# Kernel optimization log

Measured on AMD Instinct MI355X. Metric: run time of the kernel, lower is better.

Reference implementation:

```python
import jax, jax.numpy as jnp
import numpy as np

N_NODES = 100000


def _gcn_propagate(x, src, dst, n):
    """Symmetric-normalized propagation with self-loops (PyG gcn_norm, K=1).

    out[dst] += deg^-1/2[src] * deg^-1/2[dst] * x[src], including self-loops.
    """
    loop = jnp.arange(n, dtype=src.dtype)
    s = jnp.concatenate([src, loop])
    d = jnp.concatenate([dst, loop])
    deg = jax.ops.segment_sum(jnp.ones_like(d, dtype=x.dtype), d, num_segments=n)
    dinv = jnp.where(deg > 0, jax.lax.rsqrt(deg), jnp.zeros_like(deg))
    norm = dinv[s] * dinv[d]            # [E+N]
    msg = x[s] * norm[:, None]          # [E+N, F] gathered messages
    return jax.ops.segment_sum(msg, d, num_segments=n)


def setup_inputs() -> dict:
    key = jax.random.key(0)
    ks = jax.random.split(key, 6)
    n, e, f, h, c = N_NODES, 1600000, 64, 64, 16
    x = jax.random.normal(ks[0], (n, f), dtype=jnp.float32)
    edge_index = jax.random.randint(ks[1], (2, e), 0, n, dtype=jnp.int64)
    W1 = jax.random.normal(ks[2], (h, f), dtype=jnp.float32) * 0.1
    b1 = jnp.zeros((h,), dtype=jnp.float32)
    W2 = jax.random.normal(ks[3], (h, h), dtype=jnp.float32) * 0.1
    b2 = jnp.zeros((h,), dtype=jnp.float32)
    W3 = jax.random.normal(ks[4], (c, h), dtype=jnp.float32) * 0.1
    b3 = jnp.zeros((c,), dtype=jnp.float32)
    return {"x": x, "edge_index": edge_index, "W1": W1, "b1": b1,
            "W2": W2, "b2": b2, "W3": W3, "b3": b3}


def reference(x, edge_index, W1, b1, W2, b2, W3, b3):
    n = x.shape[0]
    src, dst = edge_index[0], edge_index[1]
    # SGConv 1 (K=1): propagate then linear; dropout is identity in eval mode
    h = _gcn_propagate(x, src, dst, n) @ W1.T + b1
    h = jax.nn.relu(h)
    # SGConv 2
    h = _gcn_propagate(h, src, dst, n) @ W2.T + b2
    h = jax.nn.relu(h)
    # final linear
    return h @ W3.T + b3
```

## Files before the change

kernel.cpp:

```cpp
#include <hip/hip_runtime.h>
#include <hip/hip_fp16.h>


#define F 64
#define C 16
#define SCAN_B 1024

__device__ __forceinline__ float4 ld_h4(const float2* base, size_t idx) {
    float2 raw = base[idx];
    __half2 lo = __builtin_bit_cast(__half2, raw.x);
    __half2 hi = __builtin_bit_cast(__half2, raw.y);
    float2 f0 = __half22float2(lo);
    float2 f1 = __half22float2(hi);
    return make_float4(f0.x, f0.y, f1.x, f1.y);
}

__device__ __forceinline__ float rl(float v, int l) {
    return __uint_as_float(__builtin_amdgcn_readlane(__float_as_uint(v), l));
}

__global__ void degrank_kernel(const int* __restrict__ dst, int* __restrict__ deg,
                               int* __restrict__ rank, int E) {
    int i = (blockIdx.x * blockDim.x + threadIdx.x) * 4;
    if (i + 4 <= E) {
        int4 d = *(const int4*)(dst + i);
        rank[i]     = atomicAdd(&deg[d.x], 1);
        rank[i + 1] = atomicAdd(&deg[d.y], 1);
        rank[i + 2] = atomicAdd(&deg[d.z], 1);
        rank[i + 3] = atomicAdd(&deg[d.w], 1);
    } else {
        for (int k = i; k < E; ++k) rank[k] = atomicAdd(&deg[dst[k]], 1);
    }
}

__global__ __launch_bounds__(256) void scan1_kernel(const int* __restrict__ deg,
                                                    int* __restrict__ part,
                                                    int* __restrict__ bsum, int n) {
    __shared__ int ts[256];
    int b = blockIdx.x, t = threadIdx.x;
    int base = b * SCAN_B + t * 4;
    int v[4], sum = 0;
#pragma unroll
    for (int k = 0; k < 4; ++k) { int i = base + k; v[k] = (i < n) ? deg[i] : 0; sum += v[k]; }
    ts[t] = sum;
    __syncthreads();
    for (int off = 1; off < 256; off <<= 1) {
        int add = (t >= off) ? ts[t - off] : 0;
        __syncthreads();
        ts[t] += add;
        __syncthreads();
    }
    int run = ts[t] - sum;
#pragma unroll
    for (int k = 0; k < 4; ++k) { int i = base + k; if (i < n) part[i] = run; run += v[k]; }
    if (t == 255) bsum[b] = ts[255];
}

__global__ __launch_bounds__(256) void scan2_kernel(int* __restrict__ bsum, int nb) {
    __shared__ int ts[256];
    int t = threadIdx.x;
    int v = (t < nb) ? bsum[t] : 0;
    ts[t] = v;
    __syncthreads();
    for (int off = 1; off < 256; off <<= 1) {
        int add = (t >= off) ? ts[t - off] : 0;
        __syncthreads();
        ts[t] += add;
        __syncthreads();
    }
    if (t < nb) bsum[t] = ts[t] - v;
}

__global__ void scan3_kernel(const int* __restrict__ part, const int* __restrict__ bsum,
                             const int* __restrict__ deg, int* __restrict__ rowptr,
                             float* __restrict__ dinv, int n, int E) {
    int i = blockIdx.x * blockDim.x + threadIdx.x;
    if (i < n) {
        rowptr[i] = part[i] + bsum[i / SCAN_B];
        dinv[i] = rsqrtf((float)deg[i] + 1.0f);
    }
    if (i == 0) rowptr[n] = E;
}

__global__ void fill_kernel(const int* __restrict__ src, const int* __restrict__ dst,
                            const int* __restrict__ rank, const int* __restrict__ rowptr,
                            int* __restrict__ csr_src, int E) {
    int i = (blockIdx.x * blockDim.x + threadIdx.x) * 4;
    if (i + 4 <= E) {
        int4 s = *(const int4*)(src + i);
        int4 d = *(const int4*)(dst + i);
        int4 r = *(const int4*)(rank + i);
        csr_src[rowptr[d.x] + r.x] = s.x;
        csr_src[rowptr[d.y] + r.y] = s.y;
        csr_src[rowptr[d.z] + r.z] = s.z;
        csr_src[rowptr[d.w] + r.w] = s.w;
    } else {
        for (int k = i; k < E; ++k) csr_src[rowptr[dst[k]] + rank[k]] = src[k];
    }
}

template <bool SCALE>
__global__ __launch_bounds__(256) void gemm_kernel(
    const float4* __restrict__ in4, const float* __restrict__ W,
    const float* __restrict__ scale, __half* __restrict__ yout, int n) {
    int tid = threadIdx.x;
    int lane = tid & 63;
    int m = lane & 15;
    float4 w[16];
#pragma unroll
    for (int t = 0; t < 16; ++t) w[t] = *(const float4*)(W + (size_t)lane * F + 4 * t);
    int gw = blockIdx.x * 4 + (tid >> 6);
    int nw = gridDim.x * 4;
    int node = gw;
    if (node >= n) return;
    float4 v = in4[(size_t)node * 16 + m];
    while (true) {
        int nxt = node + nw;
        float4 vn;
        if (nxt < n) vn = in4[(size_t)nxt * 16 + m];
        float acc = 0.0f;
#pragma unroll
        for (int t = 0; t < 16; ++t) {
            acc = fmaf(rl(v.x, t), w[t].x, acc);
            acc = fmaf(rl(v.y, t), w[t].y, acc);
            acc = fmaf(rl(v.z, t), w[t].z, acc);
            acc = fmaf(rl(v.w, t), w[t].w, acc);
        }
        if (SCALE) acc *= scale[node];
        yout[(size_t)node * F + lane] = __float2half(acc);
        if (nxt >= n) break;
        v = vn;
        node = nxt;
    }
}

__global__ __launch_bounds__(256) void gather1_kernel(
    const float2* __restrict__ y, const int* __restrict__ rowptr,
    const int* __restrict__ csr_src, const float* __restrict__ dinv,
    const float* __restrict__ b1, float* __restrict__ h1s, int n) {
    int tid = threadIdx.x;
    int m = tid & 15;
    float4 bias = *(const float4*)(b1 + 4 * m);
    int qid = (blockIdx.x * 256 + tid) >> 4;
    int nq = (gridDim.x * 256) >> 4;
    for (int node = qid; node < n; node += nq) {
        int beg = rowptr[node], end = rowptr[node + 1];
        float4 a0 = {0, 0, 0, 0}, a1 = {0, 0, 0, 0}, a2 = {0, 0, 0, 0}, a3 = {0, 0, 0, 0};
        int p = beg;
        for (; p + 8 <= end; p += 8) {
            int s0 = csr_src[p],     s1 = csr_src[p + 1];
            int s2 = csr_src[p + 2], s3 = csr_src[p + 3];
            int s4 = csr_src[p + 4], s5 = csr_src[p + 5];
            int s6 = csr_src[p + 6], s7 = csr_src[p + 7];
            float4 v0 = ld_h4(y, (size_t)s0 * 16 + m);
            float4 v1 = ld_h4(y, (size_t)s1 * 16 + m);
            float4 v2 = ld_h4(y, (size_t)s2 * 16 + m);
            float4 v3 = ld_h4(y, (size_t)s3 * 16 + m);
            float4 v4 = ld_h4(y, (size_t)s4 * 16 + m);
            float4 v5 = ld_h4(y, (size_t)s5 * 16 + m);
            float4 v6 = ld_h4(y, (size_t)s6 * 16 + m);
            float4 v7 = ld_h4(y, (size_t)s7 * 16 + m);
            a0.x += v0.x + v4.x; a0.y += v0.y + v4.y; a0.z += v0.z + v4.z; a0.w += v0.w + v4.w;
            a1.x += v1.x + v5.x; a1.y += v1.y + v5.y; a1.z += v1.z + v5.z; a1.w += v1.w + v5.w;
            a2.x += v2.x + v6.x; a2.y += v2.y + v6.y; a2.z += v2.z + v6.z; a2.w += v2.w + v6.w;
            a3.x += v3.x + v7.x; a3.y += v3.y + v7.y; a3.z += v3.z + v7.z; a3.w += v3.w + v7.w;
        }
        if (p + 4 <= end) {
            int s0 = csr_src[p], s1 = csr_src[p + 1], s2 = csr_src[p + 2], s3 = csr_src[p + 3];
            float4 v0 = ld_h4(y, (size_t)s0 * 16 + m);
            float4 v1 = ld_h4(y, (size_t)s1 * 16 + m);
            float4 v2 = ld_h4(y, (size_t)s2 * 16 + m);
            float4 v3 = ld_h4(y, (size_t)s3 * 16 + m);
            a0.x += v0.x; a0.y += v0.y; a0.z += v0.z; a0.w += v0.w;
            a1.x += v1.x; a1.y += v1.y; a1.z += v1.z; a1.w += v1.w;
            a2.x += v2.x; a2.y += v2.y; a2.z += v2.z; a2.w += v2.w;
            a3.x += v3.x; a3.y += v3.y; a3.z += v3.z; a3.w += v3.w;
            p += 4;
        }
        for (; p < end; ++p) {
            int s = csr_src[p];
            float4 v = ld_h4(y, (size_t)s * 16 + m);
            a0.x += v.x; a0.y += v.y; a0.z += v.z; a0.w += v.w;
        }
        a0.x += a1.x + a2.x + a3.x;
        a0.y += a1.y + a2.y + a3.y;
        a0.z += a1.z + a2.z + a3.z;
        a0.w += a1.w + a2.w + a3.w;
        float dd = dinv[node];
        float4 self = ld_h4(y, (size_t)node * 16 + m);
        float4 r;
        r.x = dd * fmaxf(fmaf(dd, a0.x + self.x, bias.x), 0.0f);
        r.y = dd * fmaxf(fmaf(dd, a0.y + self.y, bias.y), 0.0f);
        r.z = dd * fmaxf(fmaf(dd, a0.z + self.z, bias.z), 0.0f);
        r.w = dd * fmaxf(fmaf(dd, a0.w + self.w, bias.w), 0.0f);
        *(float4*)(h1s + (size_t)node * F + 4 * m) = r;
    }
}

__global__ __launch_bounds__(256) void gather2_kernel(
    const float2* __restrict__ y, const int* __restrict__ rowptr,
    const int* __restrict__ csr_src, const float* __restrict__ dinv,
    const float* __restrict__ b2, const float* __restrict__ W3,
    const float* __restrict__ b3, float* __restrict__ out, int n) {
    int tid = threadIdx.x;
    int lane = tid & 63;
    int m = lane & 15;
    int qbase = lane & 48;
    float4 bias = *(const float4*)(b2 + 4 * m);
    float b3r = b3[m];
    int qid = (blockIdx.x * 256 + tid) >> 4;
    int nq = (gridDim.x * 256) >> 4;
    for (int node = qid; node < n; node += nq) {
        int beg = rowptr[node], end = rowptr[node + 1];
        float4 a0 = {0, 0, 0, 0}, a1 = {0, 0, 0, 0}, a2 = {0, 0, 0, 0}, a3 = {0, 0, 0, 0};
        int p = beg;
        for (; p + 8 <= end; p += 8) {
            int s0 = csr_src[p],     s1 = csr_src[p + 1];
            int s2 = csr_src[p + 2], s3 = csr_src[p + 3];
            int s4 = csr_src[p + 4], s5 = csr_src[p + 5];
            int s6 = csr_src[p + 6], s7 = csr_src[p + 7];
            float4 v0 = ld_h4(y, (size_t)s0 * 16 + m);
            float4 v1 = ld_h4(y, (size_t)s1 * 16 + m);
            float4 v2 = ld_h4(y, (size_t)s2 * 16 + m);
            float4 v3 = ld_h4(y, (size_t)s3 * 16 + m);
            float4 v4 = ld_h4(y, (size_t)s4 * 16 + m);
            float4 v5 = ld_h4(y, (size_t)s5 * 16 + m);
            float4 v6 = ld_h4(y, (size_t)s6 * 16 + m);
            float4 v7 = ld_h4(y, (size_t)s7 * 16 + m);
            a0.x += v0.x + v4.x; a0.y += v0.y + v4.y; a0.z += v0.z + v4.z; a0.w += v0.w + v4.w;
            a1.x += v1.x + v5.x; a1.y += v1.y + v5.y; a1.z += v1.z + v5.z; a1.w += v1.w + v5.w;
            a2.x += v2.x + v6.x; a2.y += v2.y + v6.y; a2.z += v2.z + v6.z; a2.w += v2.w + v6.w;
            a3.x += v3.x + v7.x; a3.y += v3.y + v7.y; a3.z += v3.z + v7.z; a3.w += v3.w + v7.w;
        }
        if (p + 4 <= end) {
            int s0 = csr_src[p], s1 = csr_src[p + 1], s2 = csr_src[p + 2], s3 = csr_src[p + 3];
            float4 v0 = ld_h4(y, (size_t)s0 * 16 + m);
            float4 v1 = ld_h4(y, (size_t)s1 * 16 + m);
            float4 v2 = ld_h4(y, (size_t)s2 * 16 + m);
            float4 v3 = ld_h4(y, (size_t)s3 * 16 + m);
            a0.x += v0.x; a0.y += v0.y; a0.z += v0.z; a0.w += v0.w;
            a1.x += v1.x; a1.y += v1.y; a1.z += v1.z; a1.w += v1.w;
            a2.x += v2.x; a2.y += v2.y; a2.z += v2.z; a2.w += v2.w;
            a3.x += v3.x; a3.y += v3.y; a3.z += v3.z; a3.w += v3.w;
            p += 4;
        }
        for (; p < end; ++p) {
            int s = csr_src[p];
            float4 v = ld_h4(y, (size_t)s * 16 + m);
            a0.x += v.x; a0.y += v.y; a0.z += v.z; a0.w += v.w;
        }
        a0.x += a1.x + a2.x + a3.x;
        a0.y += a1.y + a2.y + a3.y;
        a0.z += a1.z + a2.z + a3.z;
        a0.w += a1.w + a2.w + a3.w;
        float dd = dinv[node];
        float4 self = ld_h4(y, (size_t)node * 16 + m);
        float4 h;
        h.x = fmaxf(fmaf(dd, a0.x + self.x, bias.x), 0.0f);
        h.y = fmaxf(fmaf(dd, a0.y + self.y, bias.y), 0.0f);
        h.z = fmaxf(fmaf(dd, a0.z + self.z, bias.z), 0.0f);
        h.w = fmaxf(fmaf(dd, a0.w + self.w, bias.w), 0.0f);
        float acc = 0.0f;
#pragma unroll
        for (int t = 0; t < 16; ++t) {
            float4 wv = *(const float4*)(W3 + (size_t)m * F + 4 * t);
            float hx = __shfl(h.x, qbase + t);
            float hy = __shfl(h.y, qbase + t);
            float hz = __shfl(h.z, qbase + t);
            float hw = __shfl(h.w, qbase + t);
            acc = fmaf(hx, wv.x, fmaf(hy, wv.y, fmaf(hz, wv.z, fmaf(hw, wv.w, acc))));
        }
        out[(size_t)node * C + m] = acc + b3r;
    }
}

extern "C" void kernel_launch(void* const* d_in, const int* in_sizes, int n_in,
                              void* d_out, int out_size, void* d_ws, size_t ws_size,
                              hipStream_t stream) {
    const float* x  = (const float*)d_in[0];
    const int* edge = (const int*)d_in[1];
    const float* W1 = (const float*)d_in[2];
    const float* b1 = (const float*)d_in[3];
    const float* W2 = (const float*)d_in[4];
    const float* b2 = (const float*)d_in[5];
    const float* W3 = (const float*)d_in[6];
    const float* b3 = (const float*)d_in[7];
    float* out = (float*)d_out;

    int n = in_sizes[0] / F;
    int E = in_sizes[1] / 2;
    const int* src = edge;
    const int* dst = edge + E;

    int nb = (n + SCAN_B - 1) / SCAN_B;

    char* ws = (char*)d_ws;
    size_t o = 0;
    auto alloc = [&](size_t bytes) { char* p = ws + o; o += (bytes + 255) & ~(size_t)255; return p; };
    int*    deg     = (int*)   alloc((size_t)n * 4);
    int*    rank    = (int*)   alloc((size_t)E * 4);
    int*    part    = (int*)   alloc((size_t)n * 4);
    int*    bsum    = (int*)   alloc(256 * 4);
    int*    rowptr  = (int*)   alloc((size_t)(n + 1) * 4);
    int*    csr_src = (int*)   alloc((size_t)E * 4);
    float*  dinv    = (float*) alloc((size_t)n * 4);
    __half* y1      = (__half*)alloc((size_t)n * F * 2);
    float*  h1s     = (float*) alloc((size_t)n * F * 4);
    __half* y2      = y1;

    hipMemsetAsync(deg, 0, (size_t)n * 4, stream);
    degrank_kernel<<<(E / 4 + 255) / 256, 256, 0, stream>>>(dst, deg, rank, E);

    scan1_kernel<<<nb, 256, 0, stream>>>(deg, part, bsum, n);
    scan2_kernel<<<1, 256, 0, stream>>>(bsum, nb);
    scan3_kernel<<<(n + 255) / 256, 256, 0, stream>>>(part, bsum, deg, rowptr, dinv, n, E);

    gemm_kernel<true><<<2048, 256, 0, stream>>>((const float4*)x, W1, dinv, y1, n);

    fill_kernel<<<(E / 4 + 255) / 256, 256, 0, stream>>>(src, dst, rank, rowptr, csr_src, E);

    gather1_kernel<<<2048, 256, 0, stream>>>(
        (const float2*)y1, rowptr, csr_src, dinv, b1, h1s, n);

    gemm_kernel<false><<<2048, 256, 0, stream>>>((const float4*)h1s, W2, nullptr, y2, n);

    gather2_kernel<<<2048, 256, 0, stream>>>(
        (const float2*)y2, rowptr, csr_src, dinv, b2, W3, b3, out, n);
}
```

Baseline: 283.5 us.

## Fuse second GEMM into gather2 and store layer-1 output in fp16

```diff
diff --git a/kernel.cpp b/kernel.cpp
--- a/kernel.cpp
+++ b/kernel.cpp
@@ -5,6 +5,10 @@
 #define F 64
 #define C 16
 #define SCAN_B 1024
+
+__device__ __forceinline__ float rl(float v, int l) {
+    return __uint_as_float(__builtin_amdgcn_readlane(__float_as_uint(v), l));
+}
 
 __device__ __forceinline__ float4 ld_h4(const float2* base, size_t idx) {
     float2 raw = base[idx];
@@ -13,10 +17,6 @@
     float2 f0 = __half22float2(lo);
     float2 f1 = __half22float2(hi);
     return make_float4(f0.x, f0.y, f1.x, f1.y);
-}
-
-__device__ __forceinline__ float rl(float v, int l) {
-    return __uint_as_float(__builtin_amdgcn_readlane(__float_as_uint(v), l));
 }
 
 __global__ void degrank_kernel(const int* __restrict__ dst, int* __restrict__ deg,
@@ -99,8 +99,7 @@
     }
 }
 
-template <bool SCALE>
-__global__ __launch_bounds__(256) void gemm_kernel(
+__global__ __launch_bounds__(256) void gemm1_kernel(
     const float4* __restrict__ in4, const float* __restrict__ W,
     const float* __restrict__ scale, __half* __restrict__ yout, int n) {
     int tid = threadIdx.x;
@@ -126,7 +125,7 @@
             acc = fmaf(rl(v.z, t), w[t].z, acc);
             acc = fmaf(rl(v.w, t), w[t].w, acc);
         }
-        if (SCALE) acc *= scale[node];
+        acc *= scale[node];
         yout[(size_t)node * F + lane] = __float2half(acc);
         if (nxt >= n) break;
         v = vn;
@@ -137,7 +136,7 @@
 __global__ __launch_bounds__(256) void gather1_kernel(
     const float2* __restrict__ y, const int* __restrict__ rowptr,
     const int* __restrict__ csr_src, const float* __restrict__ dinv,
-    const float* __restrict__ b1, float* __restrict__ h1s, int n) {
+    const float* __restrict__ b1, __half* __restrict__ h1s, int n) {
     int tid = threadIdx.x;
     int m = tid & 15;
     float4 bias = *(const float4*)(b1 + 4 * m);
@@ -193,25 +192,41 @@
         r.y = dd * fmaxf(fmaf(dd, a0.y + self.y, bias.y), 0.0f);
         r.z = dd * fmaxf(fmaf(dd, a0.z + self.z, bias.z), 0.0f);
         r.w = dd * fmaxf(fmaf(dd, a0.w + self.w, bias.w), 0.0f);
-        *(float4*)(h1s + (size_t)node * F + 4 * m) = r;
+        __half2 lo = __float22half2_rn(make_float2(r.x, r.y));
+        __half2 hi = __float22half2_rn(make_float2(r.z, r.w));
+        float2 packed;
+        packed.x = __builtin_bit_cast(float, lo);
+        packed.y = __builtin_bit_cast(float, hi);
+        *(float2*)(h1s + (size_t)node * F + 4 * m) = packed;
     }
 }
 
 __global__ __launch_bounds__(256) void gather2_kernel(
     const float2* __restrict__ y, const int* __restrict__ rowptr,
     const int* __restrict__ csr_src, const float* __restrict__ dinv,
-    const float* __restrict__ b2, const float* __restrict__ W3,
-    const float* __restrict__ b3, float* __restrict__ out, int n) {
+    const float* __restrict__ W2, const float* __restrict__ b2,
+    const float* __restrict__ W3, const float* __restrict__ b3,
+    float* __restrict__ out, int n) {
     int tid = threadIdx.x;
     int lane = tid & 63;
-    int m = lane & 15;
+    int q = lane >> 4, m = lane & 15;
     int qbase = lane & 48;
-    float4 bias = *(const float4*)(b2 + 4 * m);
-    float b3r = b3[m];
-    int qid = (blockIdx.x * 256 + tid) >> 4;
-    int nq = (gridDim.x * 256) >> 4;
-    for (int node = qid; node < n; node += nq) {
-        int beg = rowptr[node], end = rowptr[node + 1];
+    float4 w2[16];
+#pragma unroll
+    for (int t = 0; t < 16; ++t) w2[t] = *(const float4*)(W2 + (size_t)lane * F + 4 * t);
+    float4 w3[4];
+#pragma unroll
+    for (int t = 0; t < 4; ++t) w3[t] = *(const float4*)(W3 + (size_t)m * F + 16 * q + 4 * t);
+    float b2r = b2[lane];
+    float b3v = b3[m];
+    int wid = (blockIdx.x * 256 + tid) >> 6;
+    int nwaves = (gridDim.x * 256) >> 6;
+    for (int nb = wid * 4; nb < n; nb += nwaves * 4) {
+        int node = nb + q;
+        bool act = node < n;
+        int beg = 0, end = 0;
+        float dd = 0.0f;
+        if (act) { beg = rowptr[node]; end = rowptr[node + 1]; dd = dinv[node]; }
         float4 a0 = {0, 0, 0, 0}, a1 = {0, 0, 0, 0}, a2 = {0, 0, 0, 0}, a3 = {0, 0, 0, 0};
         int p = beg;
         for (; p + 8 <= end; p += 8) {
@@ -253,24 +268,35 @@
         a0.y += a1.y + a2.y + a3.y;
         a0.z += a1.z + a2.z + a3.z;
         a0.w += a1.w + a2.w + a3.w;
-        float dd = dinv[node];
-        float4 self = ld_h4(y, (size_t)node * 16 + m);
-        float4 h;
-        h.x = fmaxf(fmaf(dd, a0.x + self.x, bias.x), 0.0f);
-        h.y = fmaxf(fmaf(dd, a0.y + self.y, bias.y), 0.0f);
-        h.z = fmaxf(fmaf(dd, a0.z + self.z, bias.z), 0.0f);
-        h.w = fmaxf(fmaf(dd, a0.w + self.w, bias.w), 0.0f);
-        float acc = 0.0f;
-#pragma unroll
-        for (int t = 0; t < 16; ++t) {
-            float4 wv = *(const float4*)(W3 + (size_t)m * F + 4 * t);
-            float hx = __shfl(h.x, qbase + t);
-            float hy = __shfl(h.y, qbase + t);
-            float hz = __shfl(h.z, qbase + t);
-            float hw = __shfl(h.w, qbase + t);
-            acc = fmaf(hx, wv.x, fmaf(hy, wv.y, fmaf(hz, wv.z, fmaf(hw, wv.w, acc))));
-        }
-        out[(size_t)node * C + m] = acc + b3r;
+        float4 t4 = {0, 0, 0, 0};
+        if (act) {
+            float4 self = ld_h4(y, (size_t)node * 16 + m);
+            t4.x = dd * (a0.x + self.x);
+            t4.y = dd * (a0.y + self.y);
+            t4.z = dd * (a0.z + self.z);
+            t4.w = dd * (a0.w + self.w);
+        }
+#pragma unroll
+        for (int qq = 0; qq < 4; ++qq) {
+            if (nb + qq >= n) break;
+            float z = b2r;
+#pragma unroll
+            for (int tt = 0; tt < 16; ++tt) {
+                z = fmaf(rl(t4.x, 16 * qq + tt), w2[tt].x, z);
+                z = fmaf(rl(t4.y, 16 * qq + tt), w2[tt].y, z);
+                z = fmaf(rl(t4.z, 16 * qq + tt), w2[tt].z, z);
+                z = fmaf(rl(t4.w, 16 * qq + tt), w2[tt].w, z);
+            }
+            float h2 = fmaxf(z, 0.0f);
+            const float* w3f = (const float*)w3;
+            float partial = 0.0f;
+#pragma unroll
+            for (int tt = 0; tt < 16; ++tt)
+                partial = fmaf(__shfl(h2, qbase + tt), w3f[tt], partial);
+            partial += __shfl_xor(partial, 16);
+            partial += __shfl_xor(partial, 32);
+            if (lane < 16) out[(size_t)(nb + qq) * C + lane] = partial + b3v;
+        }
     }
 }
 
@@ -305,8 +331,7 @@
     int*    csr_src = (int*)   alloc((size_t)E * 4);
     float*  dinv    = (float*) alloc((size_t)n * 4);
     __half* y1      = (__half*)alloc((size_t)n * F * 2);
-    float*  h1s     = (float*) alloc((size_t)n * F * 4);
-    __half* y2      = y1;
+    __half* h1s     = (__half*)alloc((size_t)n * F * 2);
 
     hipMemsetAsync(deg, 0, (size_t)n * 4, stream);
     degrank_kernel<<<(E / 4 + 255) / 256, 256, 0, stream>>>(dst, deg, rank, E);
@@ -315,15 +340,13 @@
     scan2_kernel<<<1, 256, 0, stream>>>(bsum, nb);
     scan3_kernel<<<(n + 255) / 256, 256, 0, stream>>>(part, bsum, deg, rowptr, dinv, n, E);
 
-    gemm_kernel<true><<<2048, 256, 0, stream>>>((const float4*)x, W1, dinv, y1, n);
+    gemm1_kernel<<<2048, 256, 0, stream>>>((const float4*)x, W1, dinv, y1, n);
 
     fill_kernel<<<(E / 4 + 255) / 256, 256, 0, stream>>>(src, dst, rank, rowptr, csr_src, E);
 
     gather1_kernel<<<2048, 256, 0, stream>>>(
         (const float2*)y1, rowptr, csr_src, dinv, b1, h1s, n);
 
-    gemm_kernel<false><<<2048, 256, 0, stream>>>((const float4*)h1s, W2, nullptr, y2, n);
-
     gather2_kernel<<<2048, 256, 0, stream>>>(
-        (const float2*)y2, rowptr, csr_src, dinv, b2, W3, b3, out, n);
-}
+        (const float2*)h1s, rowptr, csr_src, dinv, W2, b2, W3, b3, out, n);
+}
```

Result: faster. 269.6 us (-4.9%).

## Split gather1 features across block pairs and store h1 in fp16

Applied to the files above, without the earlier changes.

```diff
diff --git a/kernel.cpp b/kernel.cpp
--- a/kernel.cpp
+++ b/kernel.cpp
@@ -5,6 +5,10 @@
 #define F 64
 #define C 16
 #define SCAN_B 1024
+
+__device__ __forceinline__ float rl(float v, int l) {
+    return __uint_as_float(__builtin_amdgcn_readlane(__float_as_uint(v), l));
+}
 
 __device__ __forceinline__ float4 ld_h4(const float2* base, size_t idx) {
     float2 raw = base[idx];
@@ -15,8 +19,9 @@
     return make_float4(f0.x, f0.y, f1.x, f1.y);
 }
 
-__device__ __forceinline__ float rl(float v, int l) {
-    return __uint_as_float(__builtin_amdgcn_readlane(__float_as_uint(v), l));
+__device__ __forceinline__ float2 ld_h2(const unsigned int* base, size_t idx) {
+    unsigned int raw = base[idx];
+    return __half22float2(__builtin_bit_cast(__half2, raw));
 }
 
 __global__ void degrank_kernel(const int* __restrict__ dst, int* __restrict__ deg,
@@ -99,8 +104,7 @@
     }
 }
 
-template <bool SCALE>
-__global__ __launch_bounds__(256) void gemm_kernel(
+__global__ __launch_bounds__(256) void gemm1_kernel(
     const float4* __restrict__ in4, const float* __restrict__ W,
     const float* __restrict__ scale, __half* __restrict__ yout, int n) {
     int tid = threadIdx.x;
@@ -126,7 +130,7 @@
             acc = fmaf(rl(v.z, t), w[t].z, acc);
             acc = fmaf(rl(v.w, t), w[t].w, acc);
         }
-        if (SCALE) acc *= scale[node];
+        acc *= scale[node];
         yout[(size_t)node * F + lane] = __float2half(acc);
         if (nxt >= n) break;
         v = vn;
@@ -134,66 +138,99 @@
     }
 }
 
+__global__ __launch_bounds__(256) void gemm2_kernel(
+    const float2* __restrict__ in2, const float* __restrict__ W,
+    __half* __restrict__ yout, int n) {
+    int tid = threadIdx.x;
+    int lane = tid & 63;
+    int m = lane & 15;
+    float4 w[16];
+#pragma unroll
+    for (int t = 0; t < 16; ++t) w[t] = *(const float4*)(W + (size_t)lane * F + 4 * t);
+    int gw = blockIdx.x * 4 + (tid >> 6);
+    int nw = gridDim.x * 4;
+    int node = gw;
+    if (node >= n) return;
+    float4 v = ld_h4(in2, (size_t)node * 16 + m);
+    while (true) {
+        int nxt = node + nw;
+        float4 vn;
+        if (nxt < n) vn = ld_h4(in2, (size_t)nxt * 16 + m);
+        float acc = 0.0f;
+#pragma unroll
+        for (int t = 0; t < 16; ++t) {
+            acc = fmaf(rl(v.x, t), w[t].x, acc);
+            acc = fmaf(rl(v.y, t), w[t].y, acc);
+            acc = fmaf(rl(v.z, t), w[t].z, acc);
+            acc = fmaf(rl(v.w, t), w[t].w, acc);
+        }
+        yout[(size_t)node * F + lane] = __float2half(acc);
+        if (nxt >= n) break;
+        v = vn;
+        node = nxt;
+    }
+}
+
 __global__ __launch_bounds__(256) void gather1_kernel(
-    const float2* __restrict__ y, const int* __restrict__ rowptr,
+    const unsigned int* __restrict__ y, const int* __restrict__ rowptr,
     const int* __restrict__ csr_src, const float* __restrict__ dinv,
-    const float* __restrict__ b1, float* __restrict__ h1s, int n) {
+    const float* __restrict__ b1, unsigned int* __restrict__ h1s, int n) {
     int tid = threadIdx.x;
     int m = tid & 15;
-    float4 bias = *(const float4*)(b1 + 4 * m);
-    int qid = (blockIdx.x * 256 + tid) >> 4;
-    int nq = (gridDim.x * 256) >> 4;
+    int s = blockIdx.x & 1;
+    int g = blockIdx.x >> 1;
+    int fo = 16 * s + m;
+    float2 bias = *(const float2*)(b1 + 32 * s + 2 * m);
+    int qid = g * 16 + (tid >> 4);
+    int nq = (gridDim.x >> 1) << 4;
     for (int node = qid; node < n; node += nq) {
         int beg = rowptr[node], end = rowptr[node + 1];
-        float4 a0 = {0, 0, 0, 0}, a1 = {0, 0, 0, 0}, a2 = {0, 0, 0, 0}, a3 = {0, 0, 0, 0};
+        float2 a0 = {0, 0}, a1 = {0, 0}, a2 = {0, 0}, a3 = {0, 0};
         int p = beg;
         for (; p + 8 <= end; p += 8) {
             int s0 = csr_src[p],     s1 = csr_src[p + 1];
             int s2 = csr_src[p + 2], s3 = csr_src[p + 3];
             int s4 = csr_src[p + 4], s5 = csr_src[p + 5];
             int s6 = csr_src[p + 6], s7 = csr_src[p + 7];
-            float4 v0 = ld_h4(y, (size_t)s0 * 16 + m);
-            float4 v1 = ld_h4(y, (size_t)s1 * 16 + m);
-            float4 v2 = ld_h4(y, (size_t)s2 * 16 + m);
-            float4 v3 = ld_h4(y, (size_t)s3 * 16 + m);
-            float4 v4 = ld_h4(y, (size_t)s4 * 16 + m);
-            float4 v5 = ld_h4(y, (size_t)s5 * 16 + m);
-            float4 v6 = ld_h4(y, (size_t)s6 * 16 + m);
-            float4 v7 = ld_h4(y, (size_t)s7 * 16 + m);
-            a0.x += v0.x + v4.x; a0.y += v0.y + v4.y; a0.z += v0.z + v4.z; a0.w += v0.w + v4.w;
-            a1.x += v1.x + v5.x; a1.y += v1.y + v5.y; a1.z += v1.z + v5.z; a1.w += v1.w + v5.w;
-            a2.x += v2.x + v6.x; a2.y += v2.y + v6.y; a2.z += v2.z + v6.z; a2.w += v2.w + v6.w;
-            a3.x += v3.x + v7.x; a3.y += v3.y + v7.y; a3.z += v3.z + v7.z; a3.w += v3.w + v7.w;
+            float2 v0 = ld_h2(y, (size_t)s0 * 32 + fo);
+            float2 v1 = ld_h2(y, (size_t)s1 * 32 + fo);
+            float2 v2 = ld_h2(y, (size_t)s2 * 32 + fo);
+            float2 v3 = ld_h2(y, (size_t)s3 * 32 + fo);
+            float2 v4 = ld_h2(y, (size_t)s4 * 32 + fo);
+            float2 v5 = ld_h2(y, (size_t)s5 * 32 + fo);
+            float2 v6 = ld_h2(y, (size_t)s6 * 32 + fo);
+            float2 v7 = ld_h2(y, (size_t)s7 * 32 + fo);
+            a0.x += v0.x + v4.x; a0.y += v0.y + v4.y;
+            a1.x += v1.x + v5.x; a1.y += v1.y + v5.y;
+            a2.x += v2.x + v6.x; a2.y += v2.y + v6.y;
+            a3.x += v3.x + v7.x; a3.y += v3.y + v7.y;
         }
         if (p + 4 <= end) {
             int s0 = csr_src[p], s1 = csr_src[p + 1], s2 = csr_src[p + 2], s3 = csr_src[p + 3];
-            float4 v0 = ld_h4(y, (size_t)s0 * 16 + m);
-            float4 v1 = ld_h4(y, (size_t)s1 * 16 + m);
-            float4 v2 = ld_h4(y, (size_t)s2 * 16 + m);
-            float4 v3 = ld_h4(y, (size_t)s3 * 16 + m);
-            a0.x += v0.x; a0.y += v0.y; a0.z += v0.z; a0.w += v0.w;
-            a1.x += v1.x; a1.y += v1.y; a1.z += v1.z; a1.w += v1.w;
-            a2.x += v2.x; a2.y += v2.y; a2.z += v2.z; a2.w += v2.w;
-            a3.x += v3.x; a3.y += v3.y; a3.z += v3.z; a3.w += v3.w;
+            float2 v0 = ld_h2(y, (size_t)s0 * 32 + fo);
+            float2 v1 = ld_h2(y, (size_t)s1 * 32 + fo);
+            float2 v2 = ld_h2(y, (size_t)s2 * 32 + fo);
+            float2 v3 = ld_h2(y, (size_t)s3 * 32 + fo);
+            a0.x += v0.x; a0.y += v0.y;
+            a1.x += v1.x; a1.y += v1.y;
+            a2.x += v2.x; a2.y += v2.y;
+            a3.x += v3.x; a3.y += v3.y;
             p += 4;
         }
         for (; p < end; ++p) {
-            int s = csr_src[p];
-            float4 v = ld_h4(y, (size_t)s * 16 + m);
-            a0.x += v.x; a0.y += v.y; a0.z += v.z; a0.w += v.w;
+            int sv = csr_src[p];
+            float2 v = ld_h2(y, (size_t)sv * 32 + fo);
+            a0.x += v.x; a0.y += v.y;
         }
         a0.x += a1.x + a2.x + a3.x;
         a0.y += a1.y + a2.y + a3.y;
-        a0.z += a1.z + a2.z + a3.z;
-        a0.w += a1.w + a2.w + a3.w;
         float dd = dinv[node];
-        float4 self = ld_h4(y, (size_t)node * 16 + m);
-        float4 r;
+        float2 self = ld_h2(y, (size_t)node * 32 + fo);
+        float2 r;
         r.x = dd * fmaxf(fmaf(dd, a0.x + self.x, bias.x), 0.0f);
         r.y = dd * fmaxf(fmaf(dd, a0.y + self.y, bias.y), 0.0f);
-        r.z = dd * fmaxf(fmaf(dd, a0.z + self.z, bias.z), 0.0f);
-        r.w = dd * fmaxf(fmaf(dd, a0.w + self.w, bias.w), 0.0f);
-        *(float4*)(h1s + (size_t)node * F + 4 * m) = r;
+        h1s[(size_t)node * 32 + fo] =
+            __builtin_bit_cast(unsigned int, __float22half2_rn(make_float2(r.x, r.y)));
     }
 }
 
@@ -305,7 +342,7 @@
     int*    csr_src = (int*)   alloc((size_t)E * 4);
     float*  dinv    = (float*) alloc((size_t)n * 4);
     __half* y1      = (__half*)alloc((size_t)n * F * 2);
-    float*  h1s     = (float*) alloc((size_t)n * F * 4);
+    __half* h1s     = (__half*)alloc((size_t)n * F * 2);
     __half* y2      = y1;
 
     hipMemsetAsync(deg, 0, (size_t)n * 4, stream);
@@ -315,14 +352,14 @@
     scan2_kernel<<<1, 256, 0, stream>>>(bsum, nb);
     scan3_kernel<<<(n + 255) / 256, 256, 0, stream>>>(part, bsum, deg, rowptr, dinv, n, E);
 
-    gemm_kernel<true><<<2048, 256, 0, stream>>>((const float4*)x, W1, dinv, y1, n);
+    gemm1_kernel<<<2048, 256, 0, stream>>>((const float4*)x, W1, dinv, y1, n);
 
     fill_kernel<<<(E / 4 + 255) / 256, 256, 0, stream>>>(src, dst, rank, rowptr, csr_src, E);
 
     gather1_kernel<<<2048, 256, 0, stream>>>(
-        (const float2*)y1, rowptr, csr_src, dinv, b1, h1s, n);
-
-    gemm_kernel<false><<<2048, 256, 0, stream>>>((const float4*)h1s, W2, nullptr, y2, n);
+        (const unsigned int*)y1, rowptr, csr_src, dinv, b1, (unsigned int*)h1s, n);
+
+    gemm2_kernel<<<2048, 256, 0, stream>>>((const float2*)h1s, W2, y2, n);
 
     gather2_kernel<<<2048, 256, 0, stream>>>(
         (const float2*)y2, rowptr, csr_src, dinv, b2, W3, b3, out, n);
```

New measurement: 310.0 us. 9.4% more time.
